# Performance work log

Measured on AMD Instinct MI355X. Metric: run time of the kernel, lower is better.

The kernel has to match this reference:

```python
import jax, jax.numpy as jnp
import numpy as np

TEMPERATURE = 0.07
HARD_NEG_RATIO = 0.5
NEG_INF = -9e15  # matches torch masked_fill value -9000000000000000.0


def setup_inputs() -> dict:
    key = jax.random.key(0)
    k1, k2 = jax.random.split(key)
    B, D = 4096, 128
    z1 = jax.random.normal(k1, (B, D), dtype=jnp.float32)
    z2 = jax.random.normal(k2, (B, D), dtype=jnp.float32)
    return {"z1": z1, "z2": z2}


def _l2_normalize(x, eps=1e-12):
    # F.normalize(p=2, dim=1): x / max(||x||, eps)
    n = jnp.linalg.norm(x, axis=1, keepdims=True)
    return x / jnp.maximum(n, eps)


def reference(z1, z2):
    B = z1.shape[0]
    z1n = _l2_normalize(z1)
    z2n = _l2_normalize(z2)
    z = jnp.concatenate([z1n, z2n], axis=0)  # [2B, D]
    sim = jnp.matmul(z, z.T) / TEMPERATURE   # [2B, 2B]

    # mask self-similarity on the diagonal
    eye = jnp.eye(2 * B, dtype=bool)
    sim_masked = jnp.where(eye, NEG_INF, sim)

    # positive pair similarities: row i pairs with i+B (mod 2B)
    rows = jnp.arange(2 * B)
    pos_idx = jnp.concatenate([jnp.arange(B, 2 * B), jnp.arange(0, B)])
    pos_sim = sim[rows, pos_idx]  # [2B]

    # hard negatives: top-k over masked sim (note: includes the positive, faithful to torch code)
    k = int((2 * B - 1) * HARD_NEG_RATIO)
    topk_sim, _ = jax.lax.top_k(sim_masked, k)        # [2B, k]
    hard_neg_sum = jnp.exp(topk_sim).sum(axis=1)      # [2B]

    exp_pos = jnp.exp(pos_sim)
    loss = -jnp.log(exp_pos / (exp_pos + hard_neg_sum))
    return loss.mean()
```

## Files before the change

### kernel.cpp

```cpp
#include <hip/hip_runtime.h>
#include <hip/hip_bf16.h>

#define TWO_B 8192
#define HALF_B 4096
#define DIM 128
#define RPB 32
#define THREADS 1024
#define NWAVES (THREADS / 64)
#define KTOP 4095
#define NRM_SCALE2 4.5398159f
#define LN2 0.69314718f
#define WLO (-0.28853900f)
#define WHI (0.28853900f)
#define NBINS 256
#define BIN_SCALE ((float)NBINS / (WHI - WLO))
#define INV_BIN_SCALE ((WHI - WLO) / (float)NBINS)
#define BIN_BIAS (-(WLO)*BIN_SCALE)

#define EXP2F(x) __builtin_amdgcn_exp2f(x)

typedef __bf16 bf16x8 __attribute__((ext_vector_type(8)));
typedef float f32x4 __attribute__((ext_vector_type(4)));

__global__ __launch_bounds__(256) void nrm_kernel(const float* __restrict__ z1,
                                                  const float* __restrict__ z2,
                                                  ushort* __restrict__ zb) {
    const int lane = threadIdx.x & 63;
    const int row = blockIdx.x * 4 + (threadIdx.x >> 6);
    const float* src = (row < HALF_B) ? (z1 + (size_t)row * DIM)
                                      : (z2 + (size_t)(row - HALF_B) * DIM);
    float2 v = *reinterpret_cast<const float2*>(src + lane * 2);
    float ss = v.x * v.x + v.y * v.y;
#pragma unroll
    for (int off = 32; off; off >>= 1) ss += __shfl_xor(ss, off);
    const float inv = NRM_SCALE2 / fmaxf(sqrtf(ss), 1e-12f);
    __hip_bfloat16 a = __float2bfloat16(v.x * inv);
    __hip_bfloat16 b = __float2bfloat16(v.y * inv);
    ushort2 st;
    st.x = *reinterpret_cast<ushort*>(&a);
    st.y = *reinterpret_cast<ushort*>(&b);
    *reinterpret_cast<ushort2*>(zb + (size_t)row * DIM + lane * 2) = st;
}

__global__ __launch_bounds__(THREADS) void ntxent_kernel(const ushort* __restrict__ zb,
                                                         float* __restrict__ out) {
    __shared__ unsigned cntS[RPB / 2][NBINS + 1];
    __shared__ float chunkF[RPB][16];
    __shared__ unsigned chunkC[RPB][16];
    __shared__ float sumHiS[RPB];
    __shared__ unsigned cntHiS[RPB];
    __shared__ float posS[RPB];

    const int tid = threadIdx.x;
    const int lane = tid & 63;
    const int wave = tid >> 6;
    const int rowbase = blockIdx.x * RPB;

    for (int i = tid; i < (RPB / 2) * (NBINS + 1); i += THREADS) (&cntS[0][0])[i] = 0u;
    if (tid < RPB) { sumHiS[tid] = 0.f; cntHiS[tid] = 0u; posS[tid] = 0.f; }
    __syncthreads();

    const int frow = lane & 15;
    const int kbase = (lane >> 4) * 8;
    const int drow = (lane >> 4) * 4;
    const int sp0 = rowbase, sp1 = rowbase + 16;
    const int sp2 = rowbase ^ HALF_B, sp3 = sp2 + 16;

    bf16x8 afL[4], afH[4];
    {
        const ushort* aL = zb + (size_t)(rowbase + frow) * DIM + kbase;
#pragma unroll
        for (int ks = 0; ks < 4; ++ks) {
            afL[ks] = *reinterpret_cast<const bf16x8*>(aL + ks * 32);
            afH[ks] = *reinterpret_cast<const bf16x8*>(aL + 16 * DIM + ks * 32);
        }
    }

    const ushort* zlane = zb + (size_t)frow * DIM + kbase;

#define COL16(J) (((J) >> 1) * (NWAVES * 32) + wave * 32 + (((J) & 1) << 4))

#define LOADF(DST, J)                                                            \
    {                                                                            \
        const ushort* _p = zlane + (size_t)COL16(J) * DIM;                       \
        _Pragma("unroll") for (int ks = 0; ks < 4; ++ks)                         \
            DST[ks] = *reinterpret_cast<const bf16x8*>(_p + ks * 32);            \
    }

#define MFMA8(BUF, ACCL, ACCH)                                                   \
    _Pragma("unroll") for (int ks = 0; ks < 4; ++ks) {                           \
        ACCL = __builtin_amdgcn_mfma_f32_16x16x32_bf16(afL[ks], BUF[ks], ACCL, 0, 0, 0); \
        ACCH = __builtin_amdgcn_mfma_f32_16x16x32_bf16(afH[ks], BUF[ks], ACCH, 0, 0, 0); \
    }

    unsigned cntL = 0u, cntH = 0u;
    float sHiL[4] = {0.f, 0.f, 0.f, 0.f}, sHiH[4] = {0.f, 0.f, 0.f, 0.f};

#define EPI(ACCL, ACCH, COL, CHK)                                                \
    _Pragma("unroll") for (int rg = 0; rg < 4; ++rg) {                           \
        const int growL = rowbase + drow + rg;                                   \
        const float vL = ACCL[rg];                                               \
        const float vH = ACCH[rg];                                               \
        bool useL = true, useH = true;                                           \
        if (CHK) {                                                               \
            if ((COL) == growL) useL = false;                                    \
            if ((COL) == growL + 16) useH = false;                               \
            if ((COL) == (growL ^ HALF_B)) posS[drow + rg] = vL;                 \
            if ((COL) == ((growL + 16) ^ HALF_B)) posS[drow + rg + 16] = vH;     \
        }                                                                        \
        if (useL) {                                                              \
            const float t = fmaf(vL, BIN_SCALE, BIN_BIAS);                       \
            if (t >= (float)NBINS) {                                             \
                sHiL[rg] += EXP2F(vL);                                           \
                cntL += (1u << (8 * rg));                                        \
            } else if (t >= 0.f) {                                               \
                const int bin = (int)t;                                          \
                atomicAdd(&cntS[(drow + rg) >> 1][bin], 1u << (16 * (rg & 1)));  \
            }                                                                    \
        }                                                                        \
        if (useH) {                                                              \
            const float t = fmaf(vH, BIN_SCALE, BIN_BIAS);                       \
            if (t >= (float)NBINS) {                                             \
                sHiH[rg] += EXP2F(vH);                                           \
                cntH += (1u << (8 * rg));                                        \
            } else if (t >= 0.f) {                                               \
                const int bin = (int)t;                                          \
                atomicAdd(&cntS[(drow + rg + 16) >> 1][bin], 1u << (16 * (rg & 1))); \
            }                                                                    \
        }                                                                        \
    }

#define BODY(BUF, J)                                                             \
    {                                                                            \
        f32x4 accL = {0.f, 0.f, 0.f, 0.f}, accH = {0.f, 0.f, 0.f, 0.f};          \
        MFMA8(BUF, accL, accH)                                                   \
        const int c16 = COL16(J);                                                \
        const int col = c16 + frow;                                              \
        if (c16 == sp0 || c16 == sp1 || c16 == sp2 || c16 == sp3) {              \
            EPI(accL, accH, col, true)                                           \
        } else {                                                                 \
            EPI(accL, accH, col, false)                                          \
        }                                                                        \
    }

    bf16x8 bufA[4], bufB[4];
    LOADF(bufA, 0)
    for (int j = 0; j < 32; j += 2) {
        LOADF(bufB, j + 1)
        BODY(bufA, j)
        if (j + 2 < 32) LOADF(bufA, j + 2)
        BODY(bufB, j + 1)
    }

    {
        unsigned c[8];
        float f[8];
#pragma unroll
        for (int rg = 0; rg < 4; ++rg) {
            c[rg] = (cntL >> (8 * rg)) & 0xffu;
            c[rg + 4] = (cntH >> (8 * rg)) & 0xffu;
            f[rg] = sHiL[rg];
            f[rg + 4] = sHiH[rg];
        }
#pragma unroll
        for (int r = 0; r < 8; ++r) {
#pragma unroll
            for (int s = 1; s < 16; s <<= 1) {
                c[r] += __shfl_xor(c[r], s);
                f[r] += __shfl_xor(f[r], s);
            }
        }
        if ((lane & 15) == 0) {
#pragma unroll
            for (int r = 0; r < 4; ++r) {
                atomicAdd(&cntHiS[drow + r], c[r]);
                atomicAdd(&cntHiS[drow + r + 16], c[r + 4]);
                atomicAdd(&sumHiS[drow + r], f[r]);
                atomicAdd(&sumHiS[drow + r + 16], f[r + 4]);
            }
        }
    }
    __syncthreads();

    if (tid < RPB * 16) {
        const int row = tid >> 4, c = tid & 15;
        const int btop = NBINS - 1 - c * 16;
        unsigned s = 0;
        float fs = 0.f;
#pragma unroll
        for (int t = 0; t < 16; ++t) {
            const unsigned w = cntS[row >> 1][btop - t];
            const unsigned h = (w >> (16 * (row & 1))) & 0xffffu;
            s += h;
            fs += (float)h * EXP2F(WLO + ((float)(btop - t) + 0.5f) * INV_BIN_SCALE);
        }
        chunkC[row][c] = s;
        chunkF[row][c] = fs;
    }
    __syncthreads();

    if (tid < RPB) {
        const int row = tid;
        unsigned cum = cntHiS[row];
        float fAbove = sumHiS[row];
        float radd = 0.f;
        if (cum < (unsigned)KTOP) {
            int c = 0;
            for (; c < 16; ++c) {
                const unsigned cs = chunkC[row][c];
                if (cum + cs >= (unsigned)KTOP) break;
                cum += cs;
                fAbove += chunkF[row][c];
            }
            if (c < 16) {
                const int btop = NBINS - 1 - c * 16;
                for (int t = 0; t < 16; ++t) {
                    const unsigned w = cntS[row >> 1][btop - t];
                    const unsigned h = (w >> (16 * (row & 1))) & 0xffffu;
                    const float em = EXP2F(WLO + ((float)(btop - t) + 0.5f) * INV_BIN_SCALE);
                    if (cum + h >= (unsigned)KTOP) {
                        radd = (float)(KTOP - cum) * em;
                        break;
                    }
                    cum += h;
                    fAbove += (float)h * em;
                }
            }
        }
        const float hns = fAbove + radd;
        const float wpos = posS[row];
        float loss = logf(EXP2F(wpos) + hns) - wpos * LN2;
#pragma unroll
        for (int s = 1; s < 32; s <<= 1) loss += __shfl_xor(loss, s);
        if (tid == 0) atomicAdd(out, loss * (1.0f / (float)TWO_B));
    }
}

extern "C" void kernel_launch(void* const* d_in, const int* in_sizes, int n_in,
                              void* d_out, int out_size, void* d_ws, size_t ws_size,
                              hipStream_t stream) {
    const float* z1 = (const float*)d_in[0];
    const float* z2 = (const float*)d_in[1];
    float* out = (float*)d_out;
    ushort* zb = (ushort*)d_ws;

    hipMemsetAsync(d_out, 0, sizeof(float), stream);
    nrm_kernel<<<TWO_B / 4, 256, 0, stream>>>(z1, z2, zb);
    ntxent_kernel<<<TWO_B / RPB, THREADS, 0, stream>>>(zb, out);
}
```

Baseline: 130.2 us.

## Stage column tiles into swizzled LDS via direct global-to-LDS loads

The kernel no longer has each wave load its B-operand fragments straight from global memory into registers. Instead the whole block cooperatively stages 256-column tiles of the normalized bf16 matrix into a double-buffered, XOR-swizzled LDS buffer using global_load_lds, then reads MFMA fragments from LDS. The aim is better-coalesced global traffic and overlap of the next tile's load with the current tile's MFMA and histogram epilogue. In exchange it adds a block-wide barrier per tile and about 128KB of LDS. It also gains no data reuse, because each column was already read only once per block.

```diff
diff --git a/kernel.cpp b/kernel.cpp
--- a/kernel.cpp
+++ b/kernel.cpp
@@ -7,6 +7,8 @@
 #define RPB 32
 #define THREADS 1024
 #define NWAVES (THREADS / 64)
+#define SC 256
+#define NT (TWO_B / SC)
 #define KTOP 4095
 #define NRM_SCALE2 4.5398159f
 #define LN2 0.69314718f
@@ -44,6 +46,7 @@
 
 __global__ __launch_bounds__(THREADS) void ntxent_kernel(const ushort* __restrict__ zb,
                                                          float* __restrict__ out) {
+    __shared__ ushort stageS[2][SC * DIM];
     __shared__ unsigned cntS[RPB / 2][NBINS + 1];
     __shared__ float chunkF[RPB][16];
     __shared__ unsigned chunkC[RPB][16];
@@ -58,17 +61,15 @@
 
     for (int i = tid; i < (RPB / 2) * (NBINS + 1); i += THREADS) (&cntS[0][0])[i] = 0u;
     if (tid < RPB) { sumHiS[tid] = 0.f; cntHiS[tid] = 0u; posS[tid] = 0.f; }
-    __syncthreads();
 
     const int frow = lane & 15;
-    const int kbase = (lane >> 4) * 8;
     const int drow = (lane >> 4) * 4;
     const int sp0 = rowbase, sp1 = rowbase + 16;
     const int sp2 = rowbase ^ HALF_B, sp3 = sp2 + 16;
 
     bf16x8 afL[4], afH[4];
     {
-        const ushort* aL = zb + (size_t)(rowbase + frow) * DIM + kbase;
+        const ushort* aL = zb + (size_t)(rowbase + frow) * DIM + (lane >> 4) * 8;
 #pragma unroll
         for (int ks = 0; ks < 4; ++ks) {
             afL[ks] = *reinterpret_cast<const bf16x8*>(aL + ks * 32);
@@ -76,21 +77,37 @@
         }
     }
 
-    const ushort* zlane = zb + (size_t)frow * DIM + kbase;
-
-#define COL16(J) (((J) >> 1) * (NWAVES * 32) + wave * 32 + (((J) & 1) << 4))
-
-#define LOADF(DST, J)                                                            \
-    {                                                                            \
-        const ushort* _p = zlane + (size_t)COL16(J) * DIM;                       \
-        _Pragma("unroll") for (int ks = 0; ks < 4; ++ks)                         \
-            DST[ks] = *reinterpret_cast<const bf16x8*>(_p + ks * 32);            \
-    }
-
-#define MFMA8(BUF, ACCL, ACCH)                                                   \
-    _Pragma("unroll") for (int ks = 0; ks < 4; ++ks) {                           \
-        ACCL = __builtin_amdgcn_mfma_f32_16x16x32_bf16(afL[ks], BUF[ks], ACCL, 0, 0, 0); \
-        ACCH = __builtin_amdgcn_mfma_f32_16x16x32_bf16(afH[ks], BUF[ks], ACCH, 0, 0, 0); \
+#define STAGE(BUFIDX, ST)                                                         \
+    {                                                                             \
+        const int stb = (ST) * SC;                                                \
+        _Pragma("unroll") for (int r = 0; r < 4; ++r) {                           \
+            const int o = ((r * 16 + wave) * 64 + lane) * 16;    \
+            const int colL = o >> 8;                                              \
+            const int innerp = o & 255;                                           \
+            const int src_inner = innerp ^ ((colL & 7) << 4);                     \
+            const ushort* gsrc = zb + (((size_t)(stb + colL)) << 7) + (src_inner >> 1); \
+            __builtin_amdgcn_global_load_lds(                                     \
+                (const __attribute__((address_space(1))) unsigned int*)gsrc,      \
+                (__attribute__((address_space(3))) unsigned int*)(&stageS[BUFIDX][(r * 16 + wave) * 512]), \
+                16, 0, 0);                                                        \
+        }                                                                         \
+    }
+
+#define LOADT(BUFIDX, BF)                                                         \
+    {                                                                             \
+        const int colL = wave * 16 + frow;                                        \
+        const int sw = (colL & 7) << 4;                                           \
+        const char* bp = (const char*)&stageS[BUFIDX][colL * DIM];                \
+        _Pragma("unroll") for (int ks = 0; ks < 4; ++ks) {                        \
+            const int inner = (lane >> 4) * 16 + ks * 64;              \
+            BF[ks] = *reinterpret_cast<const bf16x8*>(bp + (inner ^ sw));         \
+        }                                                                         \
+    }
+
+#define MFMA8(BF, ACCL, ACCH)                                                     \
+    _Pragma("unroll") for (int ks = 0; ks < 4; ++ks) {                            \
+        ACCL = __builtin_amdgcn_mfma_f32_16x16x32_bf16(afL[ks], BF[ks], ACCL, 0, 0, 0); \
+        ACCH = __builtin_amdgcn_mfma_f32_16x16x32_bf16(afH[ks], BF[ks], ACCH, 0, 0, 0); \
     }
 
     unsigned cntL = 0u, cntH = 0u;
@@ -130,26 +147,23 @@
         }                                                                        \
     }
 
-#define BODY(BUF, J)                                                             \
-    {                                                                            \
-        f32x4 accL = {0.f, 0.f, 0.f, 0.f}, accH = {0.f, 0.f, 0.f, 0.f};          \
-        MFMA8(BUF, accL, accH)                                                   \
-        const int c16 = COL16(J);                                                \
-        const int col = c16 + frow;                                              \
-        if (c16 == sp0 || c16 == sp1 || c16 == sp2 || c16 == sp3) {              \
-            EPI(accL, accH, col, true)                                           \
-        } else {                                                                 \
-            EPI(accL, accH, col, false)                                          \
-        }                                                                        \
-    }
-
-    bf16x8 bufA[4], bufB[4];
-    LOADF(bufA, 0)
-    for (int j = 0; j < 32; j += 2) {
-        LOADF(bufB, j + 1)
-        BODY(bufA, j)
-        if (j + 2 < 32) LOADF(bufA, j + 2)
-        BODY(bufB, j + 1)
+    STAGE(0, 0)
+    __syncthreads();
+    for (int t = 0; t < NT; ++t) {
+        const int cur = t & 1;
+        if (t + 1 < NT) STAGE(cur ^ 1, t + 1)
+        bf16x8 bfrag[4];
+        LOADT(cur, bfrag)
+        f32x4 accL = {0.f, 0.f, 0.f, 0.f}, accH = {0.f, 0.f, 0.f, 0.f};
+        MFMA8(bfrag, accL, accH)
+        const int c16 = t * SC + wave * 16;
+        const int col = c16 + frow;
+        if (c16 == sp0 || c16 == sp1 || c16 == sp2 || c16 == sp3) {
+            EPI(accL, accH, col, true)
+        } else {
+            EPI(accL, accH, col, false)
+        }
+        __syncthreads();
     }
 
     {
```

New measurement: 125.9 us. 3.3% less time.
